# Performance work log

Hardware: AMD Instinct MI355X
Metric: run time of the kernel (lower is better)

## Reference

```python
import jax, jax.numpy as jnp
import numpy as np

K = 3
STRIDE = 1
PAD = 1
IN_CH = 64
OUT_CH = 128
ALPHA = 0.5  # scaling_factor
QMAX = 127.0  # 8-bit symmetric fake quant


def fake_quant(x):
    # per-tensor symmetric 8-bit fake quant with dynamic amax + STE
    amax = jnp.max(jnp.abs(jax.lax.stop_gradient(x)))
    s = jnp.where(amax > 0, amax / QMAX, 1.0)
    q = jnp.clip(jnp.round(x / s), -QMAX, QMAX) * s
    return x + jax.lax.stop_gradient(q - x)


def im2col(x, k, stride, pad):
    # x: (B, C, H, W) -> (B, C*k*k, h_out*w_out), torch.nn.functional.unfold order (C slowest, then kh, kw)
    B, C, H, W = x.shape
    h_out = (H + 2 * pad - k) // stride + 1
    w_out = (W + 2 * pad - k) // stride + 1
    xp = jnp.pad(x, ((0, 0), (0, 0), (pad, pad), (pad, pad)))
    patches = [xp[:, :, i:i + stride * h_out:stride, j:j + stride * w_out:stride]
               for i in range(k) for j in range(k)]  # fixed k*k loop
    cols = jnp.stack(patches, axis=2)  # (B, C, k*k, h_out, w_out)
    return cols.reshape(B, C * k * k, h_out * w_out), h_out, w_out


def setup_inputs() -> dict:
    key = jax.random.key(0)
    k1, k2 = jax.random.split(key)
    inp = jax.random.normal(k1, (16, IN_CH, 128, 128), dtype=jnp.float32)
    weight = jax.random.normal(k2, (OUT_CH, IN_CH, K, K), dtype=jnp.float32) * 0.05
    return {"input": inp, "weight": weight}


def reference(input, weight):
    bs = input.shape[0]
    ksize = IN_CH * K * K
    cols, h_out, w_out = im2col(input, K, STRIDE, PAD)  # (B, ksize, L)
    num_sliding = cols.shape[2]
    x = jnp.transpose(cols, (0, 2, 1)).reshape(-1, ksize)  # (B*L, ksize)
    w_flat = weight.reshape(OUT_CH, ksize)

    act_scale = jnp.max(jnp.abs(jax.lax.stop_gradient(x)), axis=0)       # (ksize,)
    weight_scale = jnp.max(jnp.abs(jax.lax.stop_gradient(w_flat)), axis=0)  # (ksize,)
    scale = act_scale ** ALPHA / weight_scale ** (1.0 - ALPHA)
    scale = jnp.where(scale == 0, 1.0, scale)

    x = fake_quant(x / scale)
    w_flat = fake_quant(w_flat * scale)

    out = jnp.einsum('nk,ok->no', x, w_flat)  # (B*L, OUT_CH)
    out = out.reshape(bs, num_sliding, OUT_CH)
    out = jnp.transpose(out, (0, 2, 1)).reshape(bs, OUT_CH, h_out, w_out)
    return out
```

## Files before the change

kernel.cpp:

```cpp
#include <hip/hip_runtime.h>

#define BATCH 16
#define CIN   64
#define HW    128
#define OC    128
#define KSIZE 576

typedef float  float4v __attribute__((ext_vector_type(4)));
typedef short  short4v __attribute__((ext_vector_type(4)));
typedef __bf16 bfrag   __attribute__((ext_vector_type(8)));

#define WS_ACT   0
#define WS_WSC   576
#define WS_XMUL  1152
#define WS_SXSW  1728
#define WS_WQ_BYTE_OFF 8192

__device__ __forceinline__ void async_cp16(const void* g, void* l) {
    __builtin_amdgcn_global_load_lds(
        (const __attribute__((address_space(1))) unsigned int*)g,
        (__attribute__((address_space(3))) unsigned int*)l, 16, 0, 0);
}

__global__ __launch_bounds__(256) void k_absmax(const float* __restrict__ in,
                                                const float* __restrict__ w,
                                                float* __restrict__ wsf) {
    const int tid = threadIdx.x, lane = tid & 63, wid = tid >> 6;
    if (blockIdx.x < 1024) {
        const int c = blockIdx.x >> 4, bs = blockIdx.x & 15;
        const float4v* p = (const float4v*)(in + (size_t)(bs * CIN + c) * (HW * HW));
        float m[9];
#pragma unroll
        for (int i = 0; i < 9; ++i) m[i] = 0.f;
        for (int e = tid; e < 4096; e += 256) {
            const int h = e >> 5, q = e & 31;
            const float4v v = p[e];
            const float a0 = fabsf(v[0]), a1 = fabsf(v[1]), a2 = fabsf(v[2]), a3 = fabsf(v[3]);
            const float m01 = fmaxf(a0, a1), m12 = fmaxf(a1, a2);
            const float mall = fmaxf(m01, fmaxf(a2, a3));
            const float mw0 = (q == 31) ? fmaxf(m01, a2) : mall;
            const float mw2 = (q == 0)  ? fmaxf(m12, a3) : mall;
            const bool h0 = (h <= 126), h2 = (h >= 1);
            m[0] = fmaxf(m[0], h0 ? mw0 : 0.f);
            m[1] = fmaxf(m[1], h0 ? mall : 0.f);
            m[2] = fmaxf(m[2], h0 ? mw2 : 0.f);
            m[3] = fmaxf(m[3], mw0);
            m[4] = fmaxf(m[4], mall);
            m[5] = fmaxf(m[5], mw2);
            m[6] = fmaxf(m[6], h2 ? mw0 : 0.f);
            m[7] = fmaxf(m[7], h2 ? mall : 0.f);
            m[8] = fmaxf(m[8], h2 ? mw2 : 0.f);
        }
#pragma unroll
        for (int i = 0; i < 9; ++i)
            for (int off = 32; off; off >>= 1)
                m[i] = fmaxf(m[i], __shfl_down(m[i], off));
        __shared__ float sred[4][9];
        if (lane == 0)
#pragma unroll
            for (int i = 0; i < 9; ++i) sred[wid][i] = m[i];
        __syncthreads();
        if (tid < 9) {
            float mm = fmaxf(fmaxf(sred[0][tid], sred[1][tid]),
                             fmaxf(sred[2][tid], sred[3][tid]));
            atomicMax((int*)(wsf + WS_ACT + c * 9 + tid), __float_as_int(mm));
        }
    } else {
        const int k = (blockIdx.x - 1024) * 4 + wid;
        float m = fmaxf(fabsf(w[lane * KSIZE + k]), fabsf(w[(lane + 64) * KSIZE + k]));
        for (int off = 32; off; off >>= 1) m = fmaxf(m, __shfl_down(m, off));
        if (lane == 0) wsf[WS_WSC + k] = m;
    }
}

__global__ __launch_bounds__(576) void k_scale_wq(const float* __restrict__ w,
                                                  float* __restrict__ wsf,
                                                  short* __restrict__ wq_s) {
    __shared__ float ls[576];
    __shared__ float redA[9], redB[9];
    const int t = threadIdx.x, o = blockIdx.x;
    const int lane = t & 63, wid = t >> 6;
    const float a = wsf[WS_ACT + t];
    const float wv = wsf[WS_WSC + t];
    float s = sqrtf(a) / sqrtf(wv);
    if (s == 0.f) s = 1.f;
    ls[t] = s;
    float v1 = a / s;
    float v2 = wv * s;
    for (int off = 32; off; off >>= 1) {
        v1 = fmaxf(v1, __shfl_down(v1, off));
        v2 = fmaxf(v2, __shfl_down(v2, off));
    }
    if (lane == 0) { redA[wid] = v1; redB[wid] = v2; }
    __syncthreads();
    float ax = redA[0], aw = redB[0];
#pragma unroll
    for (int i = 1; i < 9; ++i) { ax = fmaxf(ax, redA[i]); aw = fmaxf(aw, redB[i]); }
    const float sx = ax > 0.f ? ax / 127.f : 1.f;
    const float sw = aw > 0.f ? aw / 127.f : 1.f;
    const int r = t >> 6, c = t & 63, ko = c * 9 + r;
    float q = rintf((w[o * KSIZE + ko] * ls[ko]) / sw);
    q = fminf(127.f, fmaxf(-127.f, q));
    wq_s[r * 8192 + o * 64 + (c ^ ((o & 7) << 3))] = (short)(__float_as_uint(q) >> 16);
    if (o == 0) {
        wsf[WS_XMUL + t] = 1.0f / (ls[ko] * sx);
        if (t == 0) wsf[WS_SXSW] = sx * sw;
    }
}

__global__ __launch_bounds__(256, 2) void k_gemm(const float* __restrict__ in,
                                                 const short* __restrict__ wq_s,
                                                 const float* __restrict__ wsf,
                                                 float* __restrict__ out) {
    __shared__ short A_l[2][128 * 72];
    __shared__ short B_l[2][128 * 64];
    const int tid = threadIdx.x;
    const int lane = tid & 63, wave = tid >> 6;
    const int b = blockIdx.x >> 7, oh = blockIdx.x & 127;
    const int wm = (wave & 1) << 6, wn = (wave >> 1) << 6;
    const float* xmul = wsf + WS_XMUL;

    float4v acc[4][4];
    const float4v zero4 = {0.f, 0.f, 0.f, 0.f};
#pragma unroll
    for (int i = 0; i < 4; ++i)
#pragma unroll
        for (int j = 0; j < 4; ++j) acc[i][j] = zero4;

    float4v Av[2][4];

    auto issue_B = [&](int r, short* Bbuf) {
        const short* src = wq_s + r * 8192 + tid * 8;
#pragma unroll
        for (int i = 0; i < 4; ++i)
            async_cp16(src + i * 2048, Bbuf + tid * 8 + i * 2048);
    };
    auto issue_A = [&](int r) {
        const int kh = r / 3;
        int h = oh + kh - 1;
        h = h < 0 ? 0 : (h > HW - 1 ? HW - 1 : h);
#pragma unroll
        for (int half = 0; half < 2; ++half) {
            const int bb = tid + half * 256;
            const int ow0 = (bb & 31) << 2, c0 = (bb >> 5) << 2;
            const float* ip = in + ((size_t)(b * CIN + c0) * HW + h) * HW + ow0;
#pragma unroll
            for (int i = 0; i < 4; ++i) Av[half][i] = *(const float4v*)(ip + i * (HW * HW));
        }
    };

    issue_A(0);
    issue_B(0, B_l[0]);

    for (int r = 0; r < 9; ++r) {
        const int buf = r & 1;
        const int kh = r / 3, kw = r - kh * 3;
        const int h = oh + kh - 1;
        const float validf = (h >= 0 && h < HW) ? 1.f : 0.f;
        short* Abuf = A_l[buf];
#pragma unroll
        for (int half = 0; half < 2; ++half) {
            const int bb = tid + half * 256;
            const int ow0 = (bb & 31) << 2, c0 = (bb >> 5) << 2;
            float4v xm = *(const float4v*)(xmul + r * 64 + c0);
#pragma unroll
            for (int i = 0; i < 4; ++i) xm[i] *= validf;
            short qs[4][4];
#pragma unroll
            for (int i = 0; i < 4; ++i)
#pragma unroll
                for (int j = 0; j < 4; ++j) {
                    float q = rintf(Av[half][i][j] * xm[i]);
                    q = fminf(127.f, fmaxf(-127.f, q));
                    qs[i][j] = (short)(__float_as_uint(q) >> 16);
                }
#pragma unroll
            for (int j = 0; j < 4; ++j) {
                const int ow = ow0 + j + 1 - kw;
                if (ow >= 0 && ow < HW) {
                    short4v pk = {qs[0][j], qs[1][j], qs[2][j], qs[3][j]};
                    const int pc = c0 ^ (((ow >> 2) & 7) << 3);
                    *(short4v*)(Abuf + ow * 72 + pc) = pk;
                }
            }
        }
        if (kw == 0 && tid < 16) {
            short4v z = {0, 0, 0, 0};
            *(short4v*)(Abuf + (tid << 2)) = z;
        }
        if (kw == 2 && tid < 16) {
            short4v z = {0, 0, 0, 0};
            *(short4v*)(Abuf + 127 * 72 + ((tid << 2) ^ 56)) = z;
        }
        __syncthreads();
        if (r < 8) {
            issue_A(r + 1);
            issue_B(r + 1, B_l[buf ^ 1]);
        }
        const short* Bbuf = B_l[buf];
#pragma unroll
        for (int ks = 0; ks < 2; ++ks) {
            const int klog = (ks << 5) + ((lane >> 4) << 3);
            bfrag af[4], bfr[4];
#pragma unroll
            for (int mt = 0; mt < 4; ++mt) {
                const int arow = wm + (mt << 4) + (lane & 15);
                const int pk2 = klog ^ (((arow >> 2) & 7) << 3);
                af[mt] = *(const bfrag*)(Abuf + arow * 72 + pk2);
            }
#pragma unroll
            for (int nt = 0; nt < 4; ++nt) {
                const int brow = wn + (nt << 4) + (lane & 15);
                const int pkb = klog ^ ((brow & 7) << 3);
                bfr[nt] = *(const bfrag*)(Bbuf + brow * 64 + pkb);
            }
#pragma unroll
            for (int mt = 0; mt < 4; ++mt)
#pragma unroll
                for (int nt = 0; nt < 4; ++nt)
                    acc[mt][nt] = __builtin_amdgcn_mfma_f32_16x16x32_bf16(
                        af[mt], bfr[nt], acc[mt][nt], 0, 0, 0);
        }
    }

    const float sxsw = wsf[WS_SXSW];
#pragma unroll
    for (int mt = 0; mt < 4; ++mt)
#pragma unroll
        for (int nt = 0; nt < 4; ++nt) {
            const int ow0 = wm + (mt << 4) + ((lane >> 4) << 2);
            const int o = wn + (nt << 4) + (lane & 15);
            float4v rv;
#pragma unroll
            for (int q = 0; q < 4; ++q) rv[q] = acc[mt][nt][q] * sxsw;
            *(float4v*)(out + ((size_t)(b * OC + o) * HW + oh) * HW + ow0) = rv;
        }
}

extern "C" void kernel_launch(void* const* d_in, const int* in_sizes, int n_in,
                              void* d_out, int out_size, void* d_ws, size_t ws_size,
                              hipStream_t stream) {
    const float* in = (const float*)d_in[0];
    const float* wt = (const float*)d_in[1];
    float* out = (float*)d_out;
    float* wsf = (float*)d_ws;
    short* wq_s = (short*)((char*)d_ws + WS_WQ_BYTE_OFF);

    k_absmax<<<dim3(1024 + 144), dim3(256), 0, stream>>>(in, wt, wsf);
    k_scale_wq<<<dim3(128), dim3(576), 0, stream>>>(wt, wsf, wq_s);
    k_gemm<<<dim3(BATCH * HW), dim3(256), 0, stream>>>(in, wq_s, wsf, out);
}
```

Measured before the change: 266.3 us.

## Switch conv GEMM to int8 MFMA with half-row tiles and XCD-aware mapping

Moves the quantized conv GEMM from bf16 MFMA to int8 MFMA (16x16x64 i8), storing the quantized weights and activations as bytes with a new swizzle. Each block now handles 64 output columns instead of a full row, gathers inputs per column directly with clamped addressing, and maps blocks so neighbouring rows stay on the same XCD. It also uses a deeper prefetch of raw activations and raises occupancy to 4 blocks per CU. The intent is to double MFMA throughput and halve LDS and weight traffic, at the cost of scalar strided global loads for activations and a more complex pipeline.

```diff
diff --git a/kernel.cpp b/kernel.cpp
--- a/kernel.cpp
+++ b/kernel.cpp
@@ -6,15 +6,17 @@
 #define OC    128
 #define KSIZE 576
 
-typedef float  float4v __attribute__((ext_vector_type(4)));
-typedef short  short4v __attribute__((ext_vector_type(4)));
-typedef __bf16 bfrag   __attribute__((ext_vector_type(8)));
+typedef float float4v __attribute__((ext_vector_type(4)));
+typedef int   int4v   __attribute__((ext_vector_type(4)));
+typedef unsigned int uint;
 
 #define WS_ACT   0
 #define WS_WSC   576
 #define WS_XMUL  1152
 #define WS_SXSW  1728
 #define WS_WQ_BYTE_OFF 8192
+
+#define SWZ(x) ((((x) & 3) ^ (((x) >> 2) & 3)))
 
 __device__ __forceinline__ void async_cp16(const void* g, void* l) {
     __builtin_amdgcn_global_load_lds(
@@ -75,7 +77,7 @@
 
 __global__ __launch_bounds__(576) void k_scale_wq(const float* __restrict__ w,
                                                   float* __restrict__ wsf,
-                                                  short* __restrict__ wq_s) {
+                                                  char* __restrict__ wq_s) {
     __shared__ float ls[576];
     __shared__ float redA[9], redB[9];
     const int t = threadIdx.x, o = blockIdx.x;
@@ -101,139 +103,133 @@
     const int r = t >> 6, c = t & 63, ko = c * 9 + r;
     float q = rintf((w[o * KSIZE + ko] * ls[ko]) / sw);
     q = fminf(127.f, fmaxf(-127.f, q));
-    wq_s[r * 8192 + o * 64 + (c ^ ((o & 7) << 3))] = (short)(__float_as_uint(q) >> 16);
+    const int qi = (int)q;
+    const int fc = c >> 4;
+    wq_s[r * 8192 + o * 64 + ((fc ^ SWZ(o)) << 4) + (c & 15)] = (char)qi;
     if (o == 0) {
         wsf[WS_XMUL + t] = 1.0f / (ls[ko] * sx);
         if (t == 0) wsf[WS_SXSW] = sx * sw;
     }
 }
 
-__global__ __launch_bounds__(256, 2) void k_gemm(const float* __restrict__ in,
-                                                 const short* __restrict__ wq_s,
+__global__ __launch_bounds__(256, 4) void k_gemm(const float* __restrict__ in,
+                                                 const char* __restrict__ wq_s,
                                                  const float* __restrict__ wsf,
                                                  float* __restrict__ out) {
-    __shared__ short A_l[2][128 * 72];
-    __shared__ short B_l[2][128 * 64];
-    const int tid = threadIdx.x;
-    const int lane = tid & 63, wave = tid >> 6;
-    const int b = blockIdx.x >> 7, oh = blockIdx.x & 127;
-    const int wm = (wave & 1) << 6, wn = (wave >> 1) << 6;
-    const float* xmul = wsf + WS_XMUL;
-
-    float4v acc[4][4];
-    const float4v zero4 = {0.f, 0.f, 0.f, 0.f};
-#pragma unroll
-    for (int i = 0; i < 4; ++i)
-#pragma unroll
-        for (int j = 0; j < 4; ++j) acc[i][j] = zero4;
-
-    float4v Av[2][4];
-
-    auto issue_B = [&](int r, short* Bbuf) {
-        const short* src = wq_s + r * 8192 + tid * 8;
-#pragma unroll
-        for (int i = 0; i < 4; ++i)
-            async_cp16(src + i * 2048, Bbuf + tid * 8 + i * 2048);
-    };
-    auto issue_A = [&](int r) {
-        const int kh = r / 3;
-        int h = oh + kh - 1;
-        h = h < 0 ? 0 : (h > HW - 1 ? HW - 1 : h);
-#pragma unroll
-        for (int half = 0; half < 2; ++half) {
-            const int bb = tid + half * 256;
-            const int ow0 = (bb & 31) << 2, c0 = (bb >> 5) << 2;
-            const float* ip = in + ((size_t)(b * CIN + c0) * HW + h) * HW + ow0;
-#pragma unroll
-            for (int i = 0; i < 4; ++i) Av[half][i] = *(const float4v*)(ip + i * (HW * HW));
-        }
-    };
-
-    issue_A(0);
-    issue_B(0, B_l[0]);
-
-    for (int r = 0; r < 9; ++r) {
-        const int buf = r & 1;
-        const int kh = r / 3, kw = r - kh * 3;
-        const int h = oh + kh - 1;
-        const float validf = (h >= 0 && h < HW) ? 1.f : 0.f;
-        short* Abuf = A_l[buf];
-#pragma unroll
-        for (int half = 0; half < 2; ++half) {
-            const int bb = tid + half * 256;
-            const int ow0 = (bb & 31) << 2, c0 = (bb >> 5) << 2;
-            float4v xm = *(const float4v*)(xmul + r * 64 + c0);
-#pragma unroll
-            for (int i = 0; i < 4; ++i) xm[i] *= validf;
-            short qs[4][4];
-#pragma unroll
-            for (int i = 0; i < 4; ++i)
-#pragma unroll
-                for (int j = 0; j < 4; ++j) {
-                    float q = rintf(Av[half][i][j] * xm[i]);
-                    q = fminf(127.f, fmaxf(-127.f, q));
-                    qs[i][j] = (short)(__float_as_uint(q) >> 16);
-                }
-#pragma unroll
-            for (int j = 0; j < 4; ++j) {
-                const int ow = ow0 + j + 1 - kw;
-                if (ow >= 0 && ow < HW) {
-                    short4v pk = {qs[0][j], qs[1][j], qs[2][j], qs[3][j]};
-                    const int pc = c0 ^ (((ow >> 2) & 7) << 3);
-                    *(short4v*)(Abuf + ow * 72 + pc) = pk;
-                }
+    __shared__ char A_l[2][64 * 80];
+    __shared__ char B_l[2][128 * 64];
+    __shared__ float xm_l[576];
+
+    const int tid = threadIdx.x, lane = tid & 63, wave = tid >> 6;
+    const int g = blockIdx.x;
+    const int xcd = g & 7, i = g >> 3;
+    const int half = i & 1;
+    const int oh = xcd * 16 + ((i >> 1) & 15);
+    const int b = i >> 5;
+    const int ow_base = half * 64;
+
+    const int wm = (wave & 1) * 32, wn = (wave >> 1) * 64;
+    const int cg = tid >> 6;
+    const int lr = tid & 63;
+    const int owd = ow_base + lr;
+
+    for (int idx = tid; idx < 144; idx += 256)
+        ((float4v*)xm_l)[idx] = ((const float4v*)(wsf + WS_XMUL))[idx];
+
+    int4v acc[2][4];
+#pragma unroll
+    for (int mt = 0; mt < 2; ++mt)
+#pragma unroll
+        for (int nt = 0; nt < 4; ++nt) acc[mt][nt] = (int4v){0, 0, 0, 0};
+
+    float Av[2][16];
+
+    auto issueA = [&](int r, float* dst) {
+        const int kh = r / 3, kw = r - 3 * kh;
+        int hh = oh + kh - 1;
+        int iw = owd - 1 + kw;
+        hh = hh < 0 ? 0 : (hh > 127 ? 127 : hh);
+        iw = iw < 0 ? 0 : (iw > 127 ? 127 : iw);
+        const float* base = in + (((size_t)(b * CIN + cg * 16) * HW + hh) * HW + iw);
+#pragma unroll
+        for (int j = 0; j < 16; ++j) dst[j] = base[j * (HW * HW)];
+    };
+
+    auto issueB = [&](int r, char* Bbuf) {
+        const char* src = wq_s + r * 8192 + tid * 16;
+        async_cp16(src, Bbuf + tid * 16);
+        async_cp16(src + 4096, Bbuf + tid * 16 + 4096);
+    };
+
+    auto quant = [&](int r, const float* src, char* Abuf) {
+        const int kh = r / 3, kw = r - 3 * kh;
+        const int hh = oh + kh - 1, iw = owd - 1 + kw;
+        const float vf = (hh >= 0 && hh < HW && iw >= 0 && iw < HW) ? 1.f : 0.f;
+        const float* xp = xm_l + r * 64 + cg * 16;
+        uint dw[4];
+#pragma unroll
+        for (int d = 0; d < 4; ++d) {
+            uint pk = 0;
+#pragma unroll
+            for (int j2 = 0; j2 < 4; ++j2) {
+                const int j = d * 4 + j2;
+                float q = rintf(src[j] * (xp[j] * vf));
+                q = fminf(127.f, fmaxf(-127.f, q));
+                pk |= ((uint)((int)q & 255)) << (8 * j2);
             }
-        }
-        if (kw == 0 && tid < 16) {
-            short4v z = {0, 0, 0, 0};
-            *(short4v*)(Abuf + (tid << 2)) = z;
-        }
-        if (kw == 2 && tid < 16) {
-            short4v z = {0, 0, 0, 0};
-            *(short4v*)(Abuf + 127 * 72 + ((tid << 2) ^ 56)) = z;
-        }
-        __syncthreads();
-        if (r < 8) {
-            issue_A(r + 1);
-            issue_B(r + 1, B_l[buf ^ 1]);
-        }
-        const short* Bbuf = B_l[buf];
-#pragma unroll
-        for (int ks = 0; ks < 2; ++ks) {
-            const int klog = (ks << 5) + ((lane >> 4) << 3);
-            bfrag af[4], bfr[4];
-#pragma unroll
-            for (int mt = 0; mt < 4; ++mt) {
-                const int arow = wm + (mt << 4) + (lane & 15);
-                const int pk2 = klog ^ (((arow >> 2) & 7) << 3);
-                af[mt] = *(const bfrag*)(Abuf + arow * 72 + pk2);
-            }
-#pragma unroll
-            for (int nt = 0; nt < 4; ++nt) {
-                const int brow = wn + (nt << 4) + (lane & 15);
-                const int pkb = klog ^ ((brow & 7) << 3);
-                bfr[nt] = *(const bfrag*)(Bbuf + brow * 64 + pkb);
-            }
-#pragma unroll
-            for (int mt = 0; mt < 4; ++mt)
-#pragma unroll
-                for (int nt = 0; nt < 4; ++nt)
-                    acc[mt][nt] = __builtin_amdgcn_mfma_f32_16x16x32_bf16(
-                        af[mt], bfr[nt], acc[mt][nt], 0, 0, 0);
-        }
+            dw[d] = pk;
+        }
+        *(uint4*)(Abuf + lr * 80 + ((cg ^ SWZ(lr)) << 4)) =
+            make_uint4(dw[0], dw[1], dw[2], dw[3]);
+    };
+
+    auto domfma = [&](const char* Abuf, const char* Bbuf) {
+        int4v af[2], bf[4];
+#pragma unroll
+        for (int mt = 0; mt < 2; ++mt) {
+            const int ar = wm + mt * 16 + (lane & 15);
+            af[mt] = *(const int4v*)(Abuf + ar * 80 + ((((lane >> 4)) ^ SWZ(ar)) << 4));
+        }
+#pragma unroll
+        for (int nt = 0; nt < 4; ++nt) {
+            const int br = wn + nt * 16 + (lane & 15);
+            bf[nt] = *(const int4v*)(Bbuf + br * 64 + ((((lane >> 4)) ^ SWZ(br)) << 4));
+        }
+#pragma unroll
+        for (int mt = 0; mt < 2; ++mt)
+#pragma unroll
+            for (int nt = 0; nt < 4; ++nt)
+                acc[mt][nt] = __builtin_amdgcn_mfma_i32_16x16x64_i8(
+                    af[mt], bf[nt], acc[mt][nt], 0, 0, 0);
+    };
+
+    issueA(0, Av[0]);
+    issueB(0, B_l[0]);
+    issueA(1, Av[1]);
+    __syncthreads();
+    quant(0, Av[0], A_l[0]);
+    __syncthreads();
+
+    for (int k = 0; k < 9; ++k) {
+        const int kb = k & 1;
+        if (k < 7) issueA(k + 2, Av[k & 1]);
+        if (k < 8) issueB(k + 1, B_l[kb ^ 1]);
+        if (k < 8) quant(k + 1, Av[(k + 1) & 1], A_l[kb ^ 1]);
+        domfma(A_l[kb], B_l[kb]);
+        if (k < 8) __syncthreads();
     }
 
     const float sxsw = wsf[WS_SXSW];
 #pragma unroll
-    for (int mt = 0; mt < 4; ++mt)
+    for (int mt = 0; mt < 2; ++mt)
 #pragma unroll
         for (int nt = 0; nt < 4; ++nt) {
-            const int ow0 = wm + (mt << 4) + ((lane >> 4) << 2);
-            const int o = wn + (nt << 4) + (lane & 15);
+            const int owp = ow_base + wm + mt * 16 + ((lane >> 4) << 2);
+            const int o = wn + nt * 16 + (lane & 15);
             float4v rv;
 #pragma unroll
-            for (int q = 0; q < 4; ++q) rv[q] = acc[mt][nt][q] * sxsw;
-            *(float4v*)(out + ((size_t)(b * OC + o) * HW + oh) * HW + ow0) = rv;
+            for (int q = 0; q < 4; ++q) rv[q] = (float)acc[mt][nt][q] * sxsw;
+            *(float4v*)(out + ((size_t)(b * OC + o) * HW + oh) * HW + owp) = rv;
         }
 }
 
@@ -244,9 +240,9 @@
     const float* wt = (const float*)d_in[1];
     float* out = (float*)d_out;
     float* wsf = (float*)d_ws;
-    short* wq_s = (short*)((char*)d_ws + WS_WQ_BYTE_OFF);
+    char* wq_s = (char*)d_ws + WS_WQ_BYTE_OFF;
 
     k_absmax<<<dim3(1024 + 144), dim3(256), 0, stream>>>(in, wt, wsf);
     k_scale_wq<<<dim3(128), dim3(576), 0, stream>>>(wt, wsf, wq_s);
-    k_gemm<<<dim3(BATCH * HW), dim3(256), 0, stream>>>(in, wq_s, wsf, out);
-}
+    k_gemm<<<dim3(4096), dim3(256), 0, stream>>>(in, wq_s, wsf, out);
+}
```

Result: slower. 286.6 us (+7.6%).
